# Kernel optimization log

Hardware: AMD Instinct MI355X
Metric: run time of the kernel (lower is better)

The kernel has to match this reference:

```python
import jax, jax.numpy as jnp
import numpy as np

AUX_LOSS_ALPHA = 0.01
TOP_K = 2
N_EXPERTS = 64


def setup_inputs() -> dict:
    key = jax.random.key(0)
    k1, k2 = jax.random.split(key)
    B, S, H, E = 4, 4096, 2048, N_EXPERTS
    hidden_states = jax.random.normal(k1, (B, S, H), dtype=jnp.float32)
    # kaiming_uniform_(a=sqrt(5)) ~ U(-1/sqrt(H), 1/sqrt(H))
    bound = 1.0 / np.sqrt(H)
    weight = jax.random.uniform(k2, (E, H), dtype=jnp.float32, minval=-bound, maxval=bound)
    return {"hidden_states": hidden_states, "weight": weight}


def reference(hidden_states, weight):
    B, S, H = hidden_states.shape
    E, K = N_EXPERTS, TOP_K
    x = hidden_states.reshape(-1, H)              # [T, H], T = B*S
    logits = jnp.einsum('th,eh->te', x, weight)   # router GEMM [T, E]
    scores = jax.nn.softmax(logits, axis=-1)
    topk_weight, topk_idx = jax.lax.top_k(scores, K)  # [T, K]
    # norm_topk_prob (K > 1)
    topk_weight = topk_weight / (jnp.sum(topk_weight, axis=-1, keepdims=True) + 1e-20)
    # seq_aux auxiliary loss (training path)
    idx2d = topk_idx.reshape(B, S * K)            # [B, S*K]
    ce = jnp.zeros((B, E), dtype=scores.dtype)
    ce = ce.at[jnp.arange(B)[:, None], idx2d].add(1.0)
    ce = ce / (S * K / E)
    scores3 = scores.reshape(B, S, E)
    aux_loss = jnp.mean(jnp.sum(ce * jnp.mean(scores3, axis=1), axis=1)) * AUX_LOSS_ALPHA
    return topk_idx, topk_weight, aux_loss
```

## Files before the change

### kernel.cpp

```cpp
#include <hip/hip_runtime.h>
#include <math.h>


#define TT 16384
#define HH 2048
#define EE 64
#define BB 4
#define TAU 2e-3f
#define NREP 8

typedef float v4f __attribute__((ext_vector_type(4)));
typedef float f4v __attribute__((ext_vector_type(4)));
typedef short s8v __attribute__((ext_vector_type(8)));

__device__ __forceinline__ unsigned short f2bf(float f) {
    unsigned u = __float_as_uint(f);
    return (unsigned short)((u + 0x7fffu + ((u >> 16) & 1u)) >> 16);
}
__device__ __forceinline__ float bf2f(unsigned short h) {
    return __uint_as_float(((unsigned)h) << 16);
}

__global__ void prep_b(const float* __restrict__ w,
                       unsigned short* __restrict__ bhi,
                       unsigned short* __restrict__ blo) {
    int idx = blockIdx.x * blockDim.x + threadIdx.x;
    int j    = idx & 7;
    int lane = (idx >> 3) & 63;
    int ks   = (idx >> 9) & 63;
    int nt   = idx >> 15;
    int e = nt * 16 + (lane & 15);
    int k = ks * 32 + (lane >> 4) * 8 + j;
    float f = w[e * HH + k];
    unsigned short h = f2bf(f);
    bhi[idx] = h;
    blo[idx] = f2bf(f - bf2f(h));
}

__global__ __launch_bounds__(256, 4) void gemm_partial(
    const float* __restrict__ x,
    const unsigned short* __restrict__ bhi, const unsigned short* __restrict__ blo,
    float* __restrict__ plog) {

    const int tid  = threadIdx.x;
    const int kseg = tid >> 6;
    const int lane = tid & 63;
    const int tok0 = blockIdx.x * 16;

    const float* __restrict__ xr =
        x + (size_t)(tok0 + (lane & 15)) * HH + kseg * 512 + (lane >> 4) * 8;
    const int ks0 = kseg * 16;

    f4v acc[4];
#pragma unroll
    for (int nt = 0; nt < 4; ++nt) acc[nt] = (f4v){0.f, 0.f, 0.f, 0.f};

    v4f a0 = *(const v4f*)xr;
    v4f a1 = *(const v4f*)(xr + 4);
    s8v bh[4], bl[4];
#pragma unroll
    for (int nt = 0; nt < 4; ++nt) {
        const size_t off = ((size_t)(nt * 64 + ks0) * 64 + lane) * 8;
        bh[nt] = *(const s8v*)&bhi[off];
        bl[nt] = *(const s8v*)&blo[off];
    }

#pragma unroll
    for (int ks = 0; ks < 16; ++ks) {
        v4f na0, na1;
        s8v nbh[4], nbl[4];
        if (ks < 15) {
            na0 = *(const v4f*)(xr + (ks + 1) * 32);
            na1 = *(const v4f*)(xr + (ks + 1) * 32 + 4);
#pragma unroll
            for (int nt = 0; nt < 4; ++nt) {
                const size_t off = ((size_t)(nt * 64 + ks0 + ks + 1) * 64 + lane) * 8;
                nbh[nt] = *(const s8v*)&bhi[off];
                nbl[nt] = *(const s8v*)&blo[off];
            }
        }
        float xs[8] = {a0.x, a0.y, a0.z, a0.w, a1.x, a1.y, a1.z, a1.w};
        s8v ah, al;
#pragma unroll
        for (int j = 0; j < 8; ++j) {
            unsigned short h = f2bf(xs[j]);
            ah[j] = (short)h;
            al[j] = (short)f2bf(xs[j] - bf2f(h));
        }
#pragma unroll
        for (int nt = 0; nt < 4; ++nt) {
            acc[nt] = __builtin_amdgcn_mfma_f32_16x16x32_bf16(ah, bh[nt], acc[nt], 0, 0, 0);
            acc[nt] = __builtin_amdgcn_mfma_f32_16x16x32_bf16(ah, bl[nt], acc[nt], 0, 0, 0);
            acc[nt] = __builtin_amdgcn_mfma_f32_16x16x32_bf16(al, bh[nt], acc[nt], 0, 0, 0);
        }
        a0 = na0; a1 = na1;
#pragma unroll
        for (int nt = 0; nt < 4; ++nt) { bh[nt] = nbh[nt]; bl[nt] = nbl[nt]; }
    }

    float* __restrict__ pout = plog + (size_t)kseg * TT * EE;
#pragma unroll
    for (int nt = 0; nt < 4; ++nt)
#pragma unroll
        for (int r = 0; r < 4; ++r)
            pout[(size_t)(tok0 + (lane >> 4) * 4 + r) * EE + nt * 16 + (lane & 15)] =
                acc[nt][r];
}

__global__ __launch_bounds__(256) void gate_topk(
    const float* __restrict__ plog,
    float* __restrict__ out_idx, float* __restrict__ out_w,
    float* __restrict__ g_cnt, float* __restrict__ g_ssum,
    int* __restrict__ wl_cnt, int* __restrict__ wl) {

    __shared__ float bssum[EE];
    const int tid  = threadIdx.x;
    const int lane = tid & 63;
    const int t    = blockIdx.x * 4 + (tid >> 6);
    const int rep  = (blockIdx.x & (NREP - 1)) * (BB * EE);

    if (tid < EE) bssum[tid] = 0.f;

    const size_t o = (size_t)t * EE + lane;
    float l = plog[o] + plog[(size_t)TT * EE + o] +
              plog[2 * (size_t)TT * EE + o] + plog[3 * (size_t)TT * EE + o];

    float mx = l;
#pragma unroll
    for (int off = 32; off; off >>= 1) mx = fmaxf(mx, __shfl_xor(mx, off, 64));
    float p = __expf(l - mx);
    float Z = p;
#pragma unroll
    for (int off = 32; off; off >>= 1) Z += __shfl_xor(Z, off, 64);
    float s = p / Z;

    float v = l;
    int cand[4]; float cl[4];
#pragma unroll
    for (int r = 0; r < 4; ++r) {
        float bv = v; int bi = lane;
#pragma unroll
        for (int off = 32; off; off >>= 1) {
            float ov = __shfl_xor(bv, off, 64);
            int   oi = __shfl_xor(bi, off, 64);
            if (ov > bv || (ov == bv && oi < bi)) { bv = ov; bi = oi; }
        }
        cand[r] = bi; cl[r] = bv;
        if (lane == bi) v = -3.4e38f;
    }

    __syncthreads();
    atomicAdd(&bssum[lane], s);

    if (lane == 0) {
        const int b = t >> 12;
        atomicAdd(&g_cnt[rep + b * EE + cand[0]], 1.f);
        atomicAdd(&g_cnt[rep + b * EE + cand[1]], 1.f);
        float w1 = 1.f / (1.f + __expf(cl[1] - cl[0]));
        out_idx[t * 2]     = (float)cand[0];
        out_idx[t * 2 + 1] = (float)cand[1];
        out_w[t * 2]       = w1;
        out_w[t * 2 + 1]   = 1.f - w1;
        if (cl[0] - cl[1] < TAU || cl[1] - cl[2] < TAU) {
            int pos = atomicAdd(wl_cnt, 1);
            wl[pos] = t;
        }
    }

    __syncthreads();
    if (tid < EE) {
        const int b0 = (blockIdx.x * 4) >> 12;
        atomicAdd(&g_ssum[rep + b0 * EE + tid], bssum[tid]);
    }
}

__global__ __launch_bounds__(256) void rerank_exact(
    const float* __restrict__ plog, const float* __restrict__ x,
    const float* __restrict__ w,
    const int* __restrict__ wl_cnt, const int* __restrict__ wl,
    float* __restrict__ out_idx, float* __restrict__ out_w) {

    const int lane = threadIdx.x & 63;
    const int wid  = blockIdx.x * 4 + (threadIdx.x >> 6);
    const int n    = wl_cnt[0];

    for (int i = wid; i < n; i += 32 * 4) {
        const int t = wl[i];
        const size_t o = (size_t)t * EE + lane;
        float l = plog[o] + plog[(size_t)TT * EE + o] +
                  plog[2 * (size_t)TT * EE + o] + plog[3 * (size_t)TT * EE + o];

        float v = l;
        int cand[4];
#pragma unroll
        for (int r = 0; r < 4; ++r) {
            float bv = v; int bi = lane;
#pragma unroll
            for (int off = 32; off; off >>= 1) {
                float ov = __shfl_xor(bv, off, 64);
                int   oi = __shfl_xor(bi, off, 64);
                if (ov > bv || (ov == bv && oi < bi)) { bv = ov; bi = oi; }
            }
            cand[r] = bi;
            if (lane == bi) v = -3.4e38f;
        }

        const float* __restrict__ xt  = x + (size_t)t * HH;
        const float* __restrict__ w0p = w + (size_t)cand[0] * HH;
        const float* __restrict__ w1p = w + (size_t)cand[1] * HH;
        const float* __restrict__ w2p = w + (size_t)cand[2] * HH;
        const float* __restrict__ w3p = w + (size_t)cand[3] * HH;
        double d0 = 0.0, d1 = 0.0, d2 = 0.0, d3 = 0.0;
#pragma unroll
        for (int ii = 0; ii < 8; ++ii) {
            const int k = ii * 256 + lane * 4;
            v4f xv = *(const v4f*)(xt + k);
            v4f a0 = *(const v4f*)(w0p + k);
            v4f a1 = *(const v4f*)(w1p + k);
            v4f a2 = *(const v4f*)(w2p + k);
            v4f a3 = *(const v4f*)(w3p + k);
            double dx0 = (double)xv.x, dx1 = (double)xv.y;
            double dx2 = (double)xv.z, dx3 = (double)xv.w;
            d0 = fma(dx0, (double)a0.x, d0); d0 = fma(dx1, (double)a0.y, d0);
            d0 = fma(dx2, (double)a0.z, d0); d0 = fma(dx3, (double)a0.w, d0);
            d1 = fma(dx0, (double)a1.x, d1); d1 = fma(dx1, (double)a1.y, d1);
            d1 = fma(dx2, (double)a1.z, d1); d1 = fma(dx3, (double)a1.w, d1);
            d2 = fma(dx0, (double)a2.x, d2); d2 = fma(dx1, (double)a2.y, d2);
            d2 = fma(dx2, (double)a2.z, d2); d2 = fma(dx3, (double)a2.w, d2);
            d3 = fma(dx0, (double)a3.x, d3); d3 = fma(dx1, (double)a3.y, d3);
            d3 = fma(dx2, (double)a3.z, d3); d3 = fma(dx3, (double)a3.w, d3);
        }
#pragma unroll
        for (int off = 32; off; off >>= 1) {
            d0 += __shfl_xor(d0, off, 64);
            d1 += __shfl_xor(d1, off, 64);
            d2 += __shfl_xor(d2, off, 64);
            d3 += __shfl_xor(d3, off, 64);
        }

        double bd[4] = {d0, d1, d2, d3};
        int e1 = cand[0]; double l1 = bd[0];
#pragma unroll
        for (int r = 1; r < 4; ++r)
            if (bd[r] > l1 || (bd[r] == l1 && cand[r] < e1)) { l1 = bd[r]; e1 = cand[r]; }
        int e2 = -1; double l2 = -1e300;
#pragma unroll
        for (int r = 0; r < 4; ++r) {
            if (cand[r] == e1) continue;
            if (e2 < 0 || bd[r] > l2 || (bd[r] == l2 && cand[r] < e2)) { l2 = bd[r]; e2 = cand[r]; }
        }

        double w1 = 1.0 / (1.0 + exp(l2 - l1));
        if (lane == 0) {
            out_idx[t * 2]     = (float)e1;
            out_idx[t * 2 + 1] = (float)e2;
            out_w[t * 2]       = (float)w1;
            out_w[t * 2 + 1]   = (float)(1.0 - w1);
        }
    }
}

__global__ void finalize(const float* __restrict__ g_cnt,
                         const float* __restrict__ g_ssum,
                         float* __restrict__ aux_out) {
    int lane = threadIdx.x;
    float a = 0.f;
    for (int b = 0; b < BB; ++b) {
        float c = 0.f, ss = 0.f;
#pragma unroll
        for (int r = 0; r < NREP; ++r) {
            c  += g_cnt[r * (BB * EE) + b * EE + lane];
            ss += g_ssum[r * (BB * EE) + b * EE + lane];
        }
        a += c * ss;
    }
#pragma unroll
    for (int off = 32; off; off >>= 1) a += __shfl_xor(a, off, 64);
    if (lane == 0) aux_out[0] = a * (0.01f / (4.f * 128.f * 4096.f));
}

extern "C" void kernel_launch(void* const* d_in, const int* in_sizes, int n_in,
                              void* d_out, int out_size, void* d_ws, size_t ws_size,
                              hipStream_t stream) {
    const float* x = (const float*)d_in[0];
    const float* w = (const float*)d_in[1];
    float* out = (float*)d_out;
    float* out_idx = out;
    float* out_w   = out + 2 * TT;
    float* aux     = out + 4 * TT;

    float* plog = (float*)d_ws;
    unsigned short* bhi = (unsigned short*)(plog + 4 * (size_t)TT * EE);
    unsigned short* blo = bhi + (size_t)EE * HH;
    float* g_cnt  = (float*)(blo + (size_t)EE * HH);
    float* g_ssum = g_cnt + NREP * BB * EE;
    int*   wl_cnt = (int*)(g_ssum + NREP * BB * EE);
    int*   wl     = wl_cnt + 16;

    hipMemsetAsync(g_cnt, 0, (2 * NREP * BB * EE + 16) * sizeof(float), stream);
    prep_b<<<(EE * HH) / 256, 256, 0, stream>>>(w, bhi, blo);
    gemm_partial<<<TT / 16, 256, 0, stream>>>(x, bhi, blo, plog);
    gate_topk<<<TT / 4, 256, 0, stream>>>(plog, out_idx, out_w,
                                          g_cnt, g_ssum, wl_cnt, wl);
    rerank_exact<<<32, 256, 0, stream>>>(plog, x, w, wl_cnt, wl, out_idx, out_w);
    finalize<<<1, 64, 0, stream>>>(g_cnt, g_ssum, aux);
}
```

Baseline: 254.2 us.

## Fuse router GEMM, gating, exact rerank and aux-loss finalize into one kernel

Merges the partial-logit GEMM, softmax/top-k gating, the fp64 rerank of near-tie tokens, and the aux-loss finalize into a single kernel. K-split partial logits are reduced in shared memory instead of through a 16 MB global workspace, and the last block (found by an atomic ticket) computes the aux loss. The memset is folded into prep_b, and the activation split switches from round-to-nearest to truncation for the high bf16 part, which is cheaper. The rerank now runs inline per flagged token, which can cause wave divergence and load imbalance, and TAU is widened so more tokens are flagged.

```diff
diff --git a/kernel.cpp b/kernel.cpp
--- a/kernel.cpp
+++ b/kernel.cpp
@@ -6,14 +6,15 @@
 #define HH 2048
 #define EE 64
 #define BB 4
-#define TAU 2e-3f
+#define TAU 3e-3f
 #define NREP 8
+#define NBLK (TT / 16)
 
 typedef float v4f __attribute__((ext_vector_type(4)));
 typedef float f4v __attribute__((ext_vector_type(4)));
 typedef short s8v __attribute__((ext_vector_type(8)));
 
-__device__ __forceinline__ unsigned short f2bf(float f) {
+__device__ __forceinline__ unsigned short f2bf_rne(float f) {
     unsigned u = __float_as_uint(f);
     return (unsigned short)((u + 0x7fffu + ((u >> 16) & 1u)) >> 16);
 }
@@ -23,7 +24,8 @@
 
 __global__ void prep_b(const float* __restrict__ w,
                        unsigned short* __restrict__ bhi,
-                       unsigned short* __restrict__ blo) {
+                       unsigned short* __restrict__ blo,
+                       float* __restrict__ gz) {
     int idx = blockIdx.x * blockDim.x + threadIdx.x;
     int j    = idx & 7;
     int lane = (idx >> 3) & 63;
@@ -32,20 +34,34 @@
     int e = nt * 16 + (lane & 15);
     int k = ks * 32 + (lane >> 4) * 8 + j;
     float f = w[e * HH + k];
-    unsigned short h = f2bf(f);
+    unsigned short h = f2bf_rne(f);
     bhi[idx] = h;
-    blo[idx] = f2bf(f - bf2f(h));
-}
-
-__global__ __launch_bounds__(256, 4) void gemm_partial(
-    const float* __restrict__ x,
+    blo[idx] = f2bf_rne(f - bf2f(h));
+    if (blockIdx.x == 0)
+        for (int i = threadIdx.x; i < 2 * NREP * BB * EE + 16; i += 256)
+            gz[i] = 0.f;
+}
+
+__global__ __launch_bounds__(256, 3) void moe_mega(
+    const float* __restrict__ x, const float* __restrict__ w,
     const unsigned short* __restrict__ bhi, const unsigned short* __restrict__ blo,
-    float* __restrict__ plog) {
+    float* __restrict__ out_idx, float* __restrict__ out_w,
+    float* __restrict__ aux_out,
+    float* __restrict__ g_cnt, float* __restrict__ g_ssum,
+    int* __restrict__ ticket) {
+
+    __shared__ float part[4][16][EE];
+    __shared__ float bssum[EE];
+    __shared__ float bcnt[EE];
+    __shared__ int lastflag;
 
     const int tid  = threadIdx.x;
     const int kseg = tid >> 6;
     const int lane = tid & 63;
     const int tok0 = blockIdx.x * 16;
+    const int b    = tok0 >> 12;
+
+    if (tid < EE) { bssum[tid] = 0.f; bcnt[tid] = 0.f; }
 
     const float* __restrict__ xr =
         x + (size_t)(tok0 + (lane & 15)) * HH + kseg * 512 + (lane >> 4) * 8;
@@ -83,9 +99,10 @@
         s8v ah, al;
 #pragma unroll
         for (int j = 0; j < 8; ++j) {
-            unsigned short h = f2bf(xs[j]);
-            ah[j] = (short)h;
-            al[j] = (short)f2bf(xs[j] - bf2f(h));
+            unsigned u = __float_as_uint(xs[j]);
+            ah[j] = (short)(u >> 16);
+            float hif = __uint_as_float(u & 0xffff0000u);
+            al[j] = (short)(__float_as_uint(xs[j] - hif) >> 16);
         }
 #pragma unroll
         for (int nt = 0; nt < 4; ++nt) {
@@ -93,105 +110,36 @@
             acc[nt] = __builtin_amdgcn_mfma_f32_16x16x32_bf16(ah, bl[nt], acc[nt], 0, 0, 0);
             acc[nt] = __builtin_amdgcn_mfma_f32_16x16x32_bf16(al, bh[nt], acc[nt], 0, 0, 0);
         }
-        a0 = na0; a1 = na1;
-#pragma unroll
-        for (int nt = 0; nt < 4; ++nt) { bh[nt] = nbh[nt]; bl[nt] = nbl[nt]; }
-    }
-
-    float* __restrict__ pout = plog + (size_t)kseg * TT * EE;
+        if (ks < 15) {
+            a0 = na0; a1 = na1;
+#pragma unroll
+            for (int nt = 0; nt < 4; ++nt) { bh[nt] = nbh[nt]; bl[nt] = nbl[nt]; }
+        }
+    }
+
 #pragma unroll
     for (int nt = 0; nt < 4; ++nt)
 #pragma unroll
         for (int r = 0; r < 4; ++r)
-            pout[(size_t)(tok0 + (lane >> 4) * 4 + r) * EE + nt * 16 + (lane & 15)] =
-                acc[nt][r];
-}
-
-__global__ __launch_bounds__(256) void gate_topk(
-    const float* __restrict__ plog,
-    float* __restrict__ out_idx, float* __restrict__ out_w,
-    float* __restrict__ g_cnt, float* __restrict__ g_ssum,
-    int* __restrict__ wl_cnt, int* __restrict__ wl) {
-
-    __shared__ float bssum[EE];
-    const int tid  = threadIdx.x;
-    const int lane = tid & 63;
-    const int t    = blockIdx.x * 4 + (tid >> 6);
-    const int rep  = (blockIdx.x & (NREP - 1)) * (BB * EE);
-
-    if (tid < EE) bssum[tid] = 0.f;
-
-    const size_t o = (size_t)t * EE + lane;
-    float l = plog[o] + plog[(size_t)TT * EE + o] +
-              plog[2 * (size_t)TT * EE + o] + plog[3 * (size_t)TT * EE + o];
-
-    float mx = l;
-#pragma unroll
-    for (int off = 32; off; off >>= 1) mx = fmaxf(mx, __shfl_xor(mx, off, 64));
-    float p = __expf(l - mx);
-    float Z = p;
-#pragma unroll
-    for (int off = 32; off; off >>= 1) Z += __shfl_xor(Z, off, 64);
-    float s = p / Z;
-
-    float v = l;
-    int cand[4]; float cl[4];
-#pragma unroll
-    for (int r = 0; r < 4; ++r) {
-        float bv = v; int bi = lane;
-#pragma unroll
-        for (int off = 32; off; off >>= 1) {
-            float ov = __shfl_xor(bv, off, 64);
-            int   oi = __shfl_xor(bi, off, 64);
-            if (ov > bv || (ov == bv && oi < bi)) { bv = ov; bi = oi; }
-        }
-        cand[r] = bi; cl[r] = bv;
-        if (lane == bi) v = -3.4e38f;
-    }
-
-    __syncthreads();
-    atomicAdd(&bssum[lane], s);
-
-    if (lane == 0) {
-        const int b = t >> 12;
-        atomicAdd(&g_cnt[rep + b * EE + cand[0]], 1.f);
-        atomicAdd(&g_cnt[rep + b * EE + cand[1]], 1.f);
-        float w1 = 1.f / (1.f + __expf(cl[1] - cl[0]));
-        out_idx[t * 2]     = (float)cand[0];
-        out_idx[t * 2 + 1] = (float)cand[1];
-        out_w[t * 2]       = w1;
-        out_w[t * 2 + 1]   = 1.f - w1;
-        if (cl[0] - cl[1] < TAU || cl[1] - cl[2] < TAU) {
-            int pos = atomicAdd(wl_cnt, 1);
-            wl[pos] = t;
-        }
-    }
-
-    __syncthreads();
-    if (tid < EE) {
-        const int b0 = (blockIdx.x * 4) >> 12;
-        atomicAdd(&g_ssum[rep + b0 * EE + tid], bssum[tid]);
-    }
-}
-
-__global__ __launch_bounds__(256) void rerank_exact(
-    const float* __restrict__ plog, const float* __restrict__ x,
-    const float* __restrict__ w,
-    const int* __restrict__ wl_cnt, const int* __restrict__ wl,
-    float* __restrict__ out_idx, float* __restrict__ out_w) {
-
-    const int lane = threadIdx.x & 63;
-    const int wid  = blockIdx.x * 4 + (threadIdx.x >> 6);
-    const int n    = wl_cnt[0];
-
-    for (int i = wid; i < n; i += 32 * 4) {
-        const int t = wl[i];
-        const size_t o = (size_t)t * EE + lane;
-        float l = plog[o] + plog[(size_t)TT * EE + o] +
-                  plog[2 * (size_t)TT * EE + o] + plog[3 * (size_t)TT * EE + o];
+            part[kseg][(lane >> 4) * 4 + r][nt * 16 + (lane & 15)] = acc[nt][r];
+    __syncthreads();
+
+    for (int ti = 0; ti < 4; ++ti) {
+        const int t = kseg * 4 + ti;
+        float l = part[0][t][lane] + part[1][t][lane] +
+                  part[2][t][lane] + part[3][t][lane];
+
+        float mx = l;
+#pragma unroll
+        for (int off = 32; off; off >>= 1) mx = fmaxf(mx, __shfl_xor(mx, off, 64));
+        float p = __expf(l - mx);
+        float Z = p;
+#pragma unroll
+        for (int off = 32; off; off >>= 1) Z += __shfl_xor(Z, off, 64);
+        atomicAdd(&bssum[lane], p / Z);
 
         float v = l;
-        int cand[4];
+        int cand[4]; float cl[4];
 #pragma unroll
         for (int r = 0; r < 4; ++r) {
             float bv = v; int bi = lane;
@@ -201,82 +149,105 @@
                 int   oi = __shfl_xor(bi, off, 64);
                 if (ov > bv || (ov == bv && oi < bi)) { bv = ov; bi = oi; }
             }
-            cand[r] = bi;
+            cand[r] = bi; cl[r] = bv;
             if (lane == bi) v = -3.4e38f;
         }
 
-        const float* __restrict__ xt  = x + (size_t)t * HH;
-        const float* __restrict__ w0p = w + (size_t)cand[0] * HH;
-        const float* __restrict__ w1p = w + (size_t)cand[1] * HH;
-        const float* __restrict__ w2p = w + (size_t)cand[2] * HH;
-        const float* __restrict__ w3p = w + (size_t)cand[3] * HH;
-        double d0 = 0.0, d1 = 0.0, d2 = 0.0, d3 = 0.0;
-#pragma unroll
-        for (int ii = 0; ii < 8; ++ii) {
-            const int k = ii * 256 + lane * 4;
-            v4f xv = *(const v4f*)(xt + k);
-            v4f a0 = *(const v4f*)(w0p + k);
-            v4f a1 = *(const v4f*)(w1p + k);
-            v4f a2 = *(const v4f*)(w2p + k);
-            v4f a3 = *(const v4f*)(w3p + k);
-            double dx0 = (double)xv.x, dx1 = (double)xv.y;
-            double dx2 = (double)xv.z, dx3 = (double)xv.w;
-            d0 = fma(dx0, (double)a0.x, d0); d0 = fma(dx1, (double)a0.y, d0);
-            d0 = fma(dx2, (double)a0.z, d0); d0 = fma(dx3, (double)a0.w, d0);
-            d1 = fma(dx0, (double)a1.x, d1); d1 = fma(dx1, (double)a1.y, d1);
-            d1 = fma(dx2, (double)a1.z, d1); d1 = fma(dx3, (double)a1.w, d1);
-            d2 = fma(dx0, (double)a2.x, d2); d2 = fma(dx1, (double)a2.y, d2);
-            d2 = fma(dx2, (double)a2.z, d2); d2 = fma(dx3, (double)a2.w, d2);
-            d3 = fma(dx0, (double)a3.x, d3); d3 = fma(dx1, (double)a3.y, d3);
-            d3 = fma(dx2, (double)a3.z, d3); d3 = fma(dx3, (double)a3.w, d3);
-        }
-#pragma unroll
-        for (int off = 32; off; off >>= 1) {
-            d0 += __shfl_xor(d0, off, 64);
-            d1 += __shfl_xor(d1, off, 64);
-            d2 += __shfl_xor(d2, off, 64);
-            d3 += __shfl_xor(d3, off, 64);
-        }
-
-        double bd[4] = {d0, d1, d2, d3};
-        int e1 = cand[0]; double l1 = bd[0];
-#pragma unroll
-        for (int r = 1; r < 4; ++r)
-            if (bd[r] > l1 || (bd[r] == l1 && cand[r] < e1)) { l1 = bd[r]; e1 = cand[r]; }
-        int e2 = -1; double l2 = -1e300;
-#pragma unroll
-        for (int r = 0; r < 4; ++r) {
-            if (cand[r] == e1) continue;
-            if (e2 < 0 || bd[r] > l2 || (bd[r] == l2 && cand[r] < e2)) { l2 = bd[r]; e2 = cand[r]; }
-        }
-
-        double w1 = 1.0 / (1.0 + exp(l2 - l1));
+        const bool flag = (cl[0] - cl[1] < TAU) || (cl[1] - cl[2] < TAU);
+        const int gt = tok0 + t;
+
         if (lane == 0) {
-            out_idx[t * 2]     = (float)e1;
-            out_idx[t * 2 + 1] = (float)e2;
-            out_w[t * 2]       = (float)w1;
-            out_w[t * 2 + 1]   = (float)(1.0 - w1);
-        }
-    }
-}
-
-__global__ void finalize(const float* __restrict__ g_cnt,
-                         const float* __restrict__ g_ssum,
-                         float* __restrict__ aux_out) {
-    int lane = threadIdx.x;
-    float a = 0.f;
-    for (int b = 0; b < BB; ++b) {
-        float c = 0.f, ss = 0.f;
-#pragma unroll
-        for (int r = 0; r < NREP; ++r) {
-            c  += g_cnt[r * (BB * EE) + b * EE + lane];
-            ss += g_ssum[r * (BB * EE) + b * EE + lane];
-        }
-        a += c * ss;
-    }
-#pragma unroll
-    for (int off = 32; off; off >>= 1) a += __shfl_xor(a, off, 64);
-    if (lane == 0) aux_out[0] = a * (0.01f / (4.f * 128.f * 4096.f));
+            atomicAdd(&bcnt[cand[0]], 1.f);
+            atomicAdd(&bcnt[cand[1]], 1.f);
+        }
+
+        if (!flag) {
+            if (lane == 0) {
+                float w1 = 1.f / (1.f + __expf(cl[1] - cl[0]));
+                out_idx[gt * 2]     = (float)cand[0];
+                out_idx[gt * 2 + 1] = (float)cand[1];
+                out_w[gt * 2]       = w1;
+                out_w[gt * 2 + 1]   = 1.f - w1;
+            }
+        } else {
+            const float* __restrict__ xt  = x + (size_t)gt * HH;
+            const float* __restrict__ w0p = w + (size_t)cand[0] * HH;
+            const float* __restrict__ w1p = w + (size_t)cand[1] * HH;
+            const float* __restrict__ w2p = w + (size_t)cand[2] * HH;
+            const float* __restrict__ w3p = w + (size_t)cand[3] * HH;
+            double d0 = 0.0, d1 = 0.0, d2 = 0.0, d3 = 0.0;
+#pragma unroll 2
+            for (int ii = 0; ii < 8; ++ii) {
+                const int k = ii * 256 + lane * 4;
+                v4f xv = *(const v4f*)(xt + k);
+                v4f q0 = *(const v4f*)(w0p + k);
+                v4f q1 = *(const v4f*)(w1p + k);
+                v4f q2 = *(const v4f*)(w2p + k);
+                v4f q3 = *(const v4f*)(w3p + k);
+                double dx0 = (double)xv.x, dx1 = (double)xv.y;
+                double dx2 = (double)xv.z, dx3 = (double)xv.w;
+                d0 = fma(dx0, (double)q0.x, d0); d0 = fma(dx1, (double)q0.y, d0);
+                d0 = fma(dx2, (double)q0.z, d0); d0 = fma(dx3, (double)q0.w, d0);
+                d1 = fma(dx0, (double)q1.x, d1); d1 = fma(dx1, (double)q1.y, d1);
+                d1 = fma(dx2, (double)q1.z, d1); d1 = fma(dx3, (double)q1.w, d1);
+                d2 = fma(dx0, (double)q2.x, d2); d2 = fma(dx1, (double)q2.y, d2);
+                d2 = fma(dx2, (double)q2.z, d2); d2 = fma(dx3, (double)q2.w, d2);
+                d3 = fma(dx0, (double)q3.x, d3); d3 = fma(dx1, (double)q3.y, d3);
+                d3 = fma(dx2, (double)q3.z, d3); d3 = fma(dx3, (double)q3.w, d3);
+            }
+#pragma unroll
+            for (int off = 32; off; off >>= 1) {
+                d0 += __shfl_xor(d0, off, 64);
+                d1 += __shfl_xor(d1, off, 64);
+                d2 += __shfl_xor(d2, off, 64);
+                d3 += __shfl_xor(d3, off, 64);
+            }
+            double bd[4] = {d0, d1, d2, d3};
+            int e1 = cand[0]; double l1 = bd[0];
+#pragma unroll
+            for (int r = 1; r < 4; ++r)
+                if (bd[r] > l1 || (bd[r] == l1 && cand[r] < e1)) { l1 = bd[r]; e1 = cand[r]; }
+            int e2 = -1; double l2 = -1e300;
+#pragma unroll
+            for (int r = 0; r < 4; ++r) {
+                if (cand[r] == e1) continue;
+                if (e2 < 0 || bd[r] > l2 || (bd[r] == l2 && cand[r] < e2)) { l2 = bd[r]; e2 = cand[r]; }
+            }
+            double w1 = 1.0 / (1.0 + exp(l2 - l1));
+            if (lane == 0) {
+                out_idx[gt * 2]     = (float)e1;
+                out_idx[gt * 2 + 1] = (float)e2;
+                out_w[gt * 2]       = (float)w1;
+                out_w[gt * 2 + 1]   = (float)(1.0 - w1);
+            }
+        }
+    }
+
+    __syncthreads();
+    const int rep = (blockIdx.x & (NREP - 1)) * (BB * EE);
+    if (tid < EE) {
+        atomicAdd(&g_ssum[rep + b * EE + tid], bssum[tid]);
+        atomicAdd(&g_cnt[rep + b * EE + tid], bcnt[tid]);
+        __threadfence();
+    }
+    __syncthreads();
+    if (tid == 0) lastflag = (atomicAdd(ticket, 1) == NBLK - 1);
+    __syncthreads();
+    if (lastflag && tid < EE) {
+        float a = 0.f;
+        for (int bb = 0; bb < BB; ++bb) {
+            float c = 0.f, ss = 0.f;
+#pragma unroll
+            for (int r = 0; r < NREP; ++r) {
+                c  += atomicAdd(&g_cnt[r * (BB * EE) + bb * EE + tid], 0.f);
+                ss += atomicAdd(&g_ssum[r * (BB * EE) + bb * EE + tid], 0.f);
+            }
+            a += c * ss;
+        }
+#pragma unroll
+        for (int off = 32; off; off >>= 1) a += __shfl_xor(a, off, 64);
+        if (tid == 0) aux_out[0] = a * (0.01f / (4.f * 128.f * 4096.f));
+    }
 }
 
 extern "C" void kernel_launch(void* const* d_in, const int* in_sizes, int n_in,
@@ -289,19 +260,13 @@
     float* out_w   = out + 2 * TT;
     float* aux     = out + 4 * TT;
 
-    float* plog = (float*)d_ws;
-    unsigned short* bhi = (unsigned short*)(plog + 4 * (size_t)TT * EE);
+    unsigned short* bhi = (unsigned short*)d_ws;
     unsigned short* blo = bhi + (size_t)EE * HH;
     float* g_cnt  = (float*)(blo + (size_t)EE * HH);
     float* g_ssum = g_cnt + NREP * BB * EE;
-    int*   wl_cnt = (int*)(g_ssum + NREP * BB * EE);
-    int*   wl     = wl_cnt + 16;
-
-    hipMemsetAsync(g_cnt, 0, (2 * NREP * BB * EE + 16) * sizeof(float), stream);
-    prep_b<<<(EE * HH) / 256, 256, 0, stream>>>(w, bhi, blo);
-    gemm_partial<<<TT / 16, 256, 0, stream>>>(x, bhi, blo, plog);
-    gate_topk<<<TT / 4, 256, 0, stream>>>(plog, out_idx, out_w,
-                                          g_cnt, g_ssum, wl_cnt, wl);
-    rerank_exact<<<32, 256, 0, stream>>>(plog, x, w, wl_cnt, wl, out_idx, out_w);
-    finalize<<<1, 64, 0, stream>>>(g_cnt, g_ssum, aux);
-}
+    int*   ticket = (int*)(g_ssum + NREP * BB * EE);
+
+    prep_b<<<(EE * HH) / 256, 256, 0, stream>>>(w, bhi, blo, g_cnt);
+    moe_mega<<<NBLK, 256, 0, stream>>>(x, w, bhi, blo, out_idx, out_w, aux,
+                                       g_cnt, g_ssum, ticket);
+}
```

Measured after the change: 249.8 us. No clear change (-1.7%).
